# Kernel tuning notes

Hardware: AMD Instinct MI355X
Metric: run time of the kernel (lower is better)

The kernel has to match this reference:

```python
import jax, jax.numpy as jnp
import numpy as np

B, S, IN, H, NC, WSEG = 2, 256, 80, 128, 40, 64
F2 = 2 * H  # bidirectional LSTM output dim


def setup_inputs() -> dict:
    key = jax.random.key(0)
    it = iter(jax.random.split(key, 48))
    def nrm(shape, scale):
        return jax.random.normal(next(it), shape, jnp.float32) * scale
    d = {}
    d["x"] = jax.random.normal(next(it), (B, S, IN), jnp.float32)
    d["lengths"] = jnp.full((B,), S, dtype=jnp.int32)
    ins = [IN, F2]
    for l in range(2):
        for dr in ("f", "b"):
            sc = 1.0 / np.sqrt(H)
            d[f"w_ih_l{l}{dr}"] = nrm((4 * H, ins[l]), sc)
            d[f"w_hh_l{l}{dr}"] = nrm((4 * H, H), sc)
            d[f"b_l{l}{dr}"] = nrm((4 * H,), sc)
    PD = 3 * F2  # pairwise phi feature dim
    d["a_s0"] = jnp.float32(0.25); d["w_s1"] = nrm((100, PD), 1.0 / np.sqrt(PD)); d["b_s1"] = jnp.zeros((100,), jnp.float32)
    d["a_s1"] = jnp.float32(0.25); d["w_s2"] = nrm((1, 100), 0.1); d["b_s2"] = jnp.zeros((1,), jnp.float32)
    d["a_c0"] = jnp.float32(0.25); d["w_c1"] = nrm((2 * NC, F2), 1.0 / np.sqrt(F2)); d["b_c1"] = jnp.zeros((2 * NC,), jnp.float32)
    d["a_c1"] = jnp.float32(0.25); d["w_c2"] = nrm((NC, 2 * NC), 0.1); d["b_c2"] = jnp.zeros((NC,), jnp.float32)
    d["a_b0"] = jnp.float32(0.25); d["w_b1"] = nrm((2 * NC, F2), 1.0 / np.sqrt(F2)); d["b_b1"] = jnp.zeros((2 * NC,), jnp.float32)
    d["a_b1"] = jnp.float32(0.25); d["w_b2"] = nrm((2, 2 * NC), 0.1); d["b_b2"] = jnp.zeros((2,), jnp.float32)
    return d


def prelu(x, a):
    return jnp.where(x >= 0, x, a * x)


def mlp(x, a0, W1, b1, a1, W2, b2):
    h = prelu(x, a0) @ W1.T + b1
    return prelu(h, a1) @ W2.T + b2


def lstm_dir(x, Wih, Whh, b, reverse):
    # PyTorch gate order: i, f, g, o
    pre = jnp.einsum("bsi,gi->sbg", x, Wih) + b  # [S,B,4H]
    if reverse:
        pre = pre[::-1]
    h0 = jnp.zeros((x.shape[0], Whh.shape[1]), x.dtype)
    def step(carry, xt):
        h, c = carry
        g = xt + h @ Whh.T
        i, f, gg, o = jnp.split(g, 4, axis=-1)
        c = jax.nn.sigmoid(f) * c + jax.nn.sigmoid(i) * jnp.tanh(gg)
        h = jax.nn.sigmoid(o) * jnp.tanh(c)
        return (h, c), h
    _, hs = jax.lax.scan(step, (h0, h0), pre)
    if reverse:
        hs = hs[::-1]
    return jnp.swapaxes(hs, 0, 1)  # [B,S,H]


def encode(x, layers):
    out = x
    for (wif, whf, bf, wib, whb, bb) in layers:
        out = jnp.concatenate([
            lstm_dir(out, wif, whf, bf, False),
            lstm_dir(out, wib, whb, bb, True),
        ], axis=-1)
    return out


def compute_scores(rnn_out, a_s0, w_s1, b_s1, a_s1, w_s2, b_s2):
    cum = jnp.cumsum(rnn_out, axis=1)
    # phi[b,i,j] = [cum[j]-cum[i], out[i], out[j]]  (faithful to calc_phi)
    c = cum[:, None, :, :] - cum[:, :, None, :]
    sh = c.shape
    dmat = jnp.broadcast_to(rnn_out[:, :, None, :], sh)
    emat = jnp.broadcast_to(rnn_out[:, None, :, :], sh)
    phi = jnp.concatenate([c, dmat, emat], axis=-1)  # [B,S,S,3*F2]
    return mlp(phi, a_s0, w_s1, b_s1, a_s1, w_s2, b_s2)[..., 0]  # [B,S,S]


def dp_backptr(scores):
    # Viterbi-style DP: best[i] = max_{j in [i-WSEG, i)} best[j] + scores[:, j, i]
    Bn, Sn = scores.shape[:2]
    def step(best, i):
        start = jnp.maximum(0, i - WSEG)
        jidx = start + jnp.arange(WSEG)
        bwin = jax.lax.dynamic_slice(best, (0, start), (Bn, WSEG))
        swin = jax.lax.dynamic_slice(scores, (0, start, i), (Bn, WSEG, 1))[..., 0]
        cand = jnp.where(jidx[None, :] < i, bwin + swin, -1e9)
        k = (start + jnp.argmax(cand, axis=1)).astype(jnp.int32)
        best = jax.lax.dynamic_update_slice(best, jnp.max(cand, axis=1, keepdims=True), (0, i))
        return best, k
    _, ks = jax.lax.scan(step, jnp.zeros((Bn, Sn), scores.dtype), jnp.arange(1, Sn))
    backptr = jnp.concatenate([jnp.zeros((1, Bn), jnp.int32), ks], axis=0).T  # [B,S]
    return backptr


def backtrack(scores, backptr, lengths):
    Bn, Sn = scores.shape[:2]
    bar = jnp.arange(Bn)
    def step(carry, _):
        cur, acc, bm = carry
        bm = bm.at[bar, cur].set(True)
        prev = backptr[bar, cur]
        active = cur > 0
        acc = acc + jnp.where(active, scores[bar, prev, cur], 0.0)
        cur = jnp.where(active, prev, 0)
        return (cur, acc, bm), None
    init = ((lengths - 1).astype(jnp.int32), jnp.zeros((Bn,), scores.dtype), jnp.zeros((Bn, Sn), bool))
    (_, acc, bm), _ = jax.lax.scan(step, init, None, length=Sn)
    return bm, acc


def reference(x, lengths,
              w_ih_l0f, w_hh_l0f, b_l0f, w_ih_l0b, w_hh_l0b, b_l0b,
              w_ih_l1f, w_hh_l1f, b_l1f, w_ih_l1b, w_hh_l1b, b_l1b,
              a_s0, w_s1, b_s1, a_s1, w_s2, b_s2,
              a_c0, w_c1, b_c1, a_c1, w_c2, b_c2,
              a_b0, w_b1, b_b1, a_b1, w_b2, b_b2):
    layers = [
        (w_ih_l0f, w_hh_l0f, b_l0f, w_ih_l0b, w_hh_l0b, b_l0b),
        (w_ih_l1f, w_hh_l1f, b_l1f, w_ih_l1b, w_hh_l1b, b_l1b),
    ]
    rnn_out = encode(x, layers)  # [B,S,2H]
    cls_out = mlp(rnn_out, a_c0, w_c1, b_c1, a_c1, w_c2, b_c2)
    bin_out = mlp(rnn_out, a_b0, w_b1, b_b1, a_b1, w_b2, b_b2)
    scores = compute_scores(rnn_out, a_s0, w_s1, b_s1, a_s1, w_s2, b_s2)
    backptr = dp_backptr(scores)
    bmask, pred_scores = backtrack(scores, backptr, lengths)
    # bmask[b,i]==1 iff i is a predicted segment boundary (padded-dense encoding of pred lists)
    return cls_out, bin_out, bmask.astype(jnp.int32), pred_scores
```

## Files before the change

### kernel.cpp

```cpp
#include <hip/hip_runtime.h>
#include <math.h>


#define OFF_BIN 20480
#define OFF_BM  21504
#define OFF_PRED 22016

__device__ __forceinline__ float preluf(float x, float a) { return x >= 0.f ? x : a * x; }
__device__ __forceinline__ float sigf(float x) { return 1.f / (1.f + __expf(-x)); }

__global__ __launch_bounds__(256) void k_pre2(const float* __restrict__ A,
                                              const float* __restrict__ B,
                                              int Adim, int K,
                                              const float* __restrict__ wf,
                                              const float* __restrict__ bf,
                                              const float* __restrict__ wb,
                                              const float* __restrict__ bb,
                                              float* __restrict__ outF,
                                              float* __restrict__ outB) {
    __shared__ __align__(16) float xs[4 * 256];
    int r0 = blockIdx.x << 2;
    int tid = threadIdx.x;
    int Bdim = K - Adim;
    for (int e = tid; e < 4 * K; e += 256) {
        int row = e / K, kk = e - row * K;
        int tb = r0 + row; int t = tb >> 1, b = tb & 1;
        float v = (kk < Adim) ? A[(size_t)((b << 8) + t) * Adim + kk]
                              : B[(size_t)((b << 8) + t) * Bdim + (kk - Adim)];
        xs[row * K + kk] = v;
    }
    __syncthreads();
    int g = tid;
    const float* w0 = wf + (size_t)g * K;
    const float* w1 = wf + (size_t)(g + 256) * K;
    const float* w2 = wb + (size_t)g * K;
    const float* w3 = wb + (size_t)(g + 256) * K;
    float acc0[4], acc1[4], acc2[4], acc3[4];
    float b0v = bf[g], b1v = bf[g + 256], b2v = bb[g], b3v = bb[g + 256];
#pragma unroll
    for (int r = 0; r < 4; ++r) { acc0[r] = b0v; acc1[r] = b1v; acc2[r] = b2v; acc3[r] = b3v; }
    for (int k = 0; k < K; k += 4) {
        float4 wq0 = *(const float4*)(w0 + k);
        float4 wq1 = *(const float4*)(w1 + k);
        float4 wq2 = *(const float4*)(w2 + k);
        float4 wq3 = *(const float4*)(w3 + k);
#pragma unroll
        for (int r = 0; r < 4; ++r) {
            float4 xq = *(const float4*)(xs + r * K + k);
            acc0[r] += wq0.x * xq.x + wq0.y * xq.y + wq0.z * xq.z + wq0.w * xq.w;
            acc1[r] += wq1.x * xq.x + wq1.y * xq.y + wq1.z * xq.z + wq1.w * xq.w;
            acc2[r] += wq2.x * xq.x + wq2.y * xq.y + wq2.z * xq.z + wq2.w * xq.w;
            acc3[r] += wq3.x * xq.x + wq3.y * xq.y + wq3.z * xq.z + wq3.w * xq.w;
        }
    }
#pragma unroll
    for (int r = 0; r < 4; ++r) {
        int tb = r0 + r;
        outF[(size_t)tb * 512 + g]       = acc0[r];
        outF[(size_t)tb * 512 + 256 + g] = acc1[r];
        outB[(size_t)tb * 512 + g]       = acc2[r];
        outB[(size_t)tb * 512 + 256 + g] = acc3[r];
    }
}

__global__ __launch_bounds__(512, 2) void k_lstm(const float* __restrict__ pre_f,
                                                 const float* __restrict__ pre_b,
                                                 const float* __restrict__ whh_f,
                                                 const float* __restrict__ whh_b,
                                                 float* __restrict__ hout_f,
                                                 float* __restrict__ hout_b) {
    const int dir = blockIdx.x >> 1;
    const int b = blockIdx.x & 1;
    const float* pre = dir ? pre_b : pre_f;
    const float* whh = dir ? whh_b : whh_f;
    float* hout = dir ? hout_b : hout_f;
    const int tid = threadIdx.x;
    const int c = tid >> 7;
    const int gg = tid & 127;
    const int k0 = c << 5;

    float w[4][32];
#pragma unroll
    for (int j = 0; j < 4; ++j) {
#pragma unroll
        for (int k = 0; k < 32; k += 4) {
            float4 v = *(const float4*)(whh + (size_t)((j << 7) + gg) * 128 + k0 + k);
            w[j][k] = v.x; w[j][k + 1] = v.y; w[j][k + 2] = v.z; w[j][k + 3] = v.w;
        }
    }

    __shared__ float hl[128];
    __shared__ float4 part[4][128];
    if (tid < 128) hl[tid] = 0.f;
    float cst = 0.f;
    __syncthreads();

    int t0 = dir ? 255 : 0;
    float p0 = 0.f, p1 = 0.f, p2 = 0.f, p3 = 0.f;
    if (tid < 128) {
        const float* pp = pre + ((size_t)t0 * 2 + b) * 512;
        p0 = pp[gg]; p1 = pp[128 + gg]; p2 = pp[256 + gg]; p3 = pp[384 + gg];
    }

    for (int step = 0; step < 256; ++step) {
        int t = dir ? (255 - step) : step;
        float n0 = 0.f, n1 = 0.f, n2 = 0.f, n3 = 0.f;
        if (step < 255 && tid < 128) {
            int tn = dir ? (254 - step) : (step + 1);
            const float* pp = pre + ((size_t)tn * 2 + b) * 512;
            n0 = pp[gg]; n1 = pp[128 + gg]; n2 = pp[256 + gg]; n3 = pp[384 + gg];
        }
        float a0 = 0.f, a1 = 0.f, a2 = 0.f, a3 = 0.f;
#pragma unroll
        for (int k = 0; k < 32; k += 4) {
            float4 h4 = *(const float4*)(hl + k0 + k);
            a0 += w[0][k] * h4.x + w[0][k + 1] * h4.y + w[0][k + 2] * h4.z + w[0][k + 3] * h4.w;
            a1 += w[1][k] * h4.x + w[1][k + 1] * h4.y + w[1][k + 2] * h4.z + w[1][k + 3] * h4.w;
            a2 += w[2][k] * h4.x + w[2][k + 1] * h4.y + w[2][k + 2] * h4.z + w[2][k + 3] * h4.w;
            a3 += w[3][k] * h4.x + w[3][k + 1] * h4.y + w[3][k + 2] * h4.z + w[3][k + 3] * h4.w;
        }
        part[c][gg] = make_float4(a0, a1, a2, a3);
        __syncthreads();
        if (tid < 128) {
            float4 q0 = part[0][gg], q1 = part[1][gg], q2 = part[2][gg], q3 = part[3][gg];
            float gi = p0 + ((q0.x + q1.x) + (q2.x + q3.x));
            float gf = p1 + ((q0.y + q1.y) + (q2.y + q3.y));
            float gG = p2 + ((q0.z + q1.z) + (q2.z + q3.z));
            float go = p3 + ((q0.w + q1.w) + (q2.w + q3.w));
            cst = sigf(gf) * cst + sigf(gi) * tanhf(gG);
            float h = sigf(go) * tanhf(cst);
            hl[gg] = h;
            hout[(size_t)(((b << 8) + t) << 7) + gg] = h;
            p0 = n0; p1 = n1; p2 = n2; p3 = n3;
        }
        __syncthreads();
    }
}

__global__ __launch_bounds__(256) void k_cum(const float* __restrict__ h1f,
                                             const float* __restrict__ h1b,
                                             float* __restrict__ rnn,
                                             float* __restrict__ cum) {
    int b = blockIdx.x, k = threadIdx.x;
    const float* src = (k < 128) ? h1f : h1b;
    int kk = k & 127;
    float run = 0.f;
#pragma unroll 8
    for (int t = 0; t < 256; ++t) {
        float v = src[(size_t)(((b << 8) + t) << 7) + kk];
        size_t o = (size_t)(((b << 8) + t) << 8) + k;
        rnn[o] = v;
        run += v;
        cum[o] = run;
    }
}

__global__ __launch_bounds__(256) void k_pde(const float* __restrict__ rnn,
                                             const float* __restrict__ ws1,
                                             const float* __restrict__ bs1,
                                             const float* __restrict__ a_s0,
                                             float* __restrict__ Pd,
                                             float* __restrict__ Pe) {
    int row = blockIdx.x;
    __shared__ __align__(16) float pr[256];
    float a0 = a_s0[0];
    float v = rnn[(size_t)row * 256 + threadIdx.x];
    pr[threadIdx.x] = preluf(v, a0);
    __syncthreads();
    int t = threadIdx.x;
    const float4* p4 = (const float4*)pr;
    if (t < 100) {
        const float4* wr = (const float4*)(ws1 + (size_t)t * 768 + 256);
        float acc = bs1[t];
#pragma unroll 8
        for (int q = 0; q < 64; ++q) {
            float4 w4 = wr[q], x4 = p4[q];
            acc += w4.x * x4.x + w4.y * x4.y + w4.z * x4.z + w4.w * x4.w;
        }
        Pd[(size_t)row * 100 + t] = acc;
    } else if (t >= 128 && t < 228) {
        int u = t - 128;
        const float4* wr = (const float4*)(ws1 + (size_t)u * 768 + 512);
        float acc = 0.f;
#pragma unroll 8
        for (int q = 0; q < 64; ++q) {
            float4 w4 = wr[q], x4 = p4[q];
            acc += w4.x * x4.x + w4.y * x4.y + w4.z * x4.z + w4.w * x4.w;
        }
        Pe[(size_t)row * 100 + u] = acc;
    }
}

__global__ __launch_bounds__(256) void k_head(const float* __restrict__ rnn,
                                              const float* ac0p, const float* __restrict__ wc1,
                                              const float* __restrict__ bc1, const float* ac1p,
                                              const float* __restrict__ wc2, const float* __restrict__ bc2,
                                              const float* ab0p, const float* __restrict__ wb1,
                                              const float* __restrict__ bb1, const float* ab1p,
                                              const float* __restrict__ wb2, const float* __restrict__ bb2,
                                              float* __restrict__ out) {
    int row = blockIdx.x;
    int tid = threadIdx.x;
    __shared__ __align__(16) float xc[256];
    __shared__ __align__(16) float xb[256];
    __shared__ __align__(16) float hc[80];
    __shared__ __align__(16) float hb[80];
    float ac0 = ac0p[0], ac1 = ac1p[0], ab0 = ab0p[0], ab1 = ab1p[0];
    float v = rnn[(size_t)row * 256 + tid];
    xc[tid] = preluf(v, ac0);
    xb[tid] = preluf(v, ab0);
    __syncthreads();
    if (tid < 80) {
        const float4* wr = (const float4*)(wc1 + (size_t)tid * 256);
        const float4* x4 = (const float4*)xc;
        float acc = bc1[tid];
#pragma unroll 8
        for (int q = 0; q < 64; ++q) {
            float4 w4 = wr[q], p = x4[q];
            acc += w4.x * p.x + w4.y * p.y + w4.z * p.z + w4.w * p.w;
        }
        hc[tid] = preluf(acc, ac1);
    } else if (tid >= 128 && tid < 208) {
        int u = tid - 128;
        const float4* wr = (const float4*)(wb1 + (size_t)u * 256);
        const float4* x4 = (const float4*)xb;
        float acc = bb1[u];
#pragma unroll 8
        for (int q = 0; q < 64; ++q) {
            float4 w4 = wr[q], p = x4[q];
            acc += w4.x * p.x + w4.y * p.y + w4.z * p.z + w4.w * p.w;
        }
        hb[u] = preluf(acc, ab1);
    }
    __syncthreads();
    if (tid < 40) {
        const float4* wr = (const float4*)(wc2 + (size_t)tid * 80);
        const float4* h4 = (const float4*)hc;
        float acc = bc2[tid];
#pragma unroll
        for (int q = 0; q < 20; ++q) {
            float4 w4 = wr[q], p = h4[q];
            acc += w4.x * p.x + w4.y * p.y + w4.z * p.z + w4.w * p.w;
        }
        out[(size_t)row * 40 + tid] = acc;
    } else if (tid >= 64 && tid < 66) {
        int j = tid - 64;
        const float4* wr = (const float4*)(wb2 + (size_t)j * 80);
        const float4* h4 = (const float4*)hb;
        float acc = bb2[j];
#pragma unroll
        for (int q = 0; q < 20; ++q) {
            float4 w4 = wr[q], p = h4[q];
            acc += w4.x * p.x + w4.y * p.y + w4.z * p.z + w4.w * p.w;
        }
        out[OFF_BIN + (size_t)row * 2 + j] = acc;
    }
}

__global__ __launch_bounds__(256) void k_scores(const float* __restrict__ cum,
                                                const float* __restrict__ ws1,
                                                const float* __restrict__ ws2,
                                                const float* __restrict__ bs2,
                                                const float* __restrict__ Pd,
                                                const float* __restrict__ Pe,
                                                const float* a_s0p, const float* a_s1p,
                                                float* __restrict__ scT) {
    int bid = blockIdx.x;
    int dt = bid & 3, e = (bid >> 2) & 255, b = bid >> 10;
    int d0 = dt << 6;
    int tid = threadIdx.x;
    __shared__ float cume[256];
    __shared__ float Y[64 * 257];
    __shared__ float red[4][64];
    float a0 = a_s0p[0], a1 = a_s1p[0];
    cume[tid] = cum[(size_t)(((b << 8) + e) << 8) + tid];
    __syncthreads();
#pragma unroll 4
    for (int dj = 0; dj < 64; ++dj) {
        float cd = cum[(size_t)(((b << 8) + (d0 + dj)) << 8) + tid];
        Y[dj * 257 + tid] = preluf(cume[tid] - cd, a0);
    }
    __syncthreads();
    int ug = __builtin_amdgcn_readfirstlane(tid >> 6);
    int ld = tid & 63;
    int d = d0 + ld;
    float acc[25];
#pragma unroll
    for (int t = 0; t < 25; ++t) acc[t] = 0.f;
    const float* wc = ws1 + (size_t)(ug * 25) * 768;
    const float* yrow = Y + ld * 257;
    for (int k = 0; k < 256; k += 4) {
        float y0 = yrow[k], y1 = yrow[k + 1], y2 = yrow[k + 2], y3 = yrow[k + 3];
#pragma unroll
        for (int t = 0; t < 25; ++t) {
            float4 wq = *(const float4*)(wc + (size_t)t * 768 + k);
            acc[t] += y0 * wq.x + y1 * wq.y + y2 * wq.z + y3 * wq.w;
        }
    }
    const float* pdrow = Pd + (size_t)((b << 8) + d) * 100;
    const float* perow = Pe + (size_t)((b << 8) + e) * 100;
    float part = 0.f;
#pragma unroll
    for (int t = 0; t < 25; ++t) {
        int u = ug * 25 + t;
        float h = acc[t] + pdrow[u] + perow[u];
        part += preluf(h, a1) * ws2[u];
    }
    red[ug][ld] = part;
    __syncthreads();
    if (tid < 64) {
        float s = red[0][tid] + red[1][tid] + red[2][tid] + red[3][tid] + bs2[0];
        scT[(size_t)(((b << 8) + e) << 8) + d0 + tid] = s;
    }
}

__global__ __launch_bounds__(128) void k_dp(const float* __restrict__ scT,
                                            const int* __restrict__ lengths,
                                            float* __restrict__ out) {
    __shared__ float best[2][256];
    __shared__ int bp[2][256];
    __shared__ float bm[2][256];
    int tid = threadIdx.x;
    for (int i = tid; i < 512; i += 128) {
        ((float*)best)[i] = 0.f;
        ((int*)bp)[i] = 0;
        ((float*)bm)[i] = 0.f;
    }
    __syncthreads();
    int b = tid >> 6, ln = tid & 63;
    const float* sb = scT + ((size_t)b << 16);
    float sc_next = sb[(1 << 8) + ln];
    for (int i = 1; i < 256; ++i) {
        float sc = sc_next;
        if (i < 255) {
            int i2 = i + 1;
            int st2 = (i2 > 64) ? (i2 - 64) : 0;
            sc_next = sb[(i2 << 8) + st2 + ln];
        }
        int start = (i > 64) ? (i - 64) : 0;
        int j = start + ln;
        float v = -1000000000.0f;
        int ki = j;
        if (j < i) v = best[b][j] + sc;
#pragma unroll
        for (int off = 32; off > 0; off >>= 1) {
            float ov = __shfl_down(v, off);
            int ok = __shfl_down(ki, off);
            if (ov > v || (ov == v && ok < ki)) { v = ov; ki = ok; }
        }
        if (ln == 0) { best[b][i] = v; bp[b][i] = ki; }
    }
    __syncthreads();
    if (tid < 2) {
        int bb = tid;
        int cur = lengths[bb] - 1;
        out[OFF_PRED + bb] = best[bb][cur];
        for (int it = 0; it < 256; ++it) {
            bm[bb][cur] = 1.f;
            int prev = bp[bb][cur];
            cur = (cur > 0) ? prev : 0;
        }
    }
    __syncthreads();
    for (int i = tid; i < 512; i += 128) out[OFF_BM + i] = ((float*)bm)[i];
}

extern "C" void kernel_launch(void* const* d_in, const int* in_sizes, int n_in,
                              void* d_out, int out_size, void* d_ws, size_t ws_size,
                              hipStream_t stream) {
    const float* x     = (const float*)d_in[0];
    const int* lengths = (const int*)d_in[1];
    const float* wih0f = (const float*)d_in[2];
    const float* whh0f = (const float*)d_in[3];
    const float* b0f   = (const float*)d_in[4];
    const float* wih0b = (const float*)d_in[5];
    const float* whh0b = (const float*)d_in[6];
    const float* b0b   = (const float*)d_in[7];
    const float* wih1f = (const float*)d_in[8];
    const float* whh1f = (const float*)d_in[9];
    const float* b1f   = (const float*)d_in[10];
    const float* wih1b = (const float*)d_in[11];
    const float* whh1b = (const float*)d_in[12];
    const float* b1b   = (const float*)d_in[13];
    const float* a_s0  = (const float*)d_in[14];
    const float* w_s1  = (const float*)d_in[15];
    const float* b_s1  = (const float*)d_in[16];
    const float* a_s1  = (const float*)d_in[17];
    const float* w_s2  = (const float*)d_in[18];
    const float* b_s2  = (const float*)d_in[19];
    const float* a_c0  = (const float*)d_in[20];
    const float* w_c1  = (const float*)d_in[21];
    const float* b_c1  = (const float*)d_in[22];
    const float* a_c1  = (const float*)d_in[23];
    const float* w_c2  = (const float*)d_in[24];
    const float* b_c2  = (const float*)d_in[25];
    const float* a_b0  = (const float*)d_in[26];
    const float* w_b1  = (const float*)d_in[27];
    const float* b_b1  = (const float*)d_in[28];
    const float* a_b1  = (const float*)d_in[29];
    const float* w_b2  = (const float*)d_in[30];
    const float* b_b2  = (const float*)d_in[31];

    float* wsf = (float*)d_ws;
    float* preF = wsf;
    float* preB = wsf + 262144;
    float* h0f  = wsf + 524288;
    float* h0b  = wsf + 589824;
    float* h1f  = wsf + 655360;
    float* h1b  = wsf + 720896;
    float* rnn  = wsf + 786432;
    float* cum  = wsf + 917504;
    float* Pd   = wsf + 1048576;
    float* Pe   = wsf + 1099776;
    float* scT  = wsf + 1150976;
    float* out  = (float*)d_out;

    k_pre2<<<128, 256, 0, stream>>>(x, x, 80, 80, wih0f, b0f, wih0b, b0b, preF, preB);
    k_lstm<<<4, 512, 0, stream>>>(preF, preB, whh0f, whh0b, h0f, h0b);
    k_pre2<<<128, 256, 0, stream>>>(h0f, h0b, 128, 256, wih1f, b1f, wih1b, b1b, preF, preB);
    k_lstm<<<4, 512, 0, stream>>>(preF, preB, whh1f, whh1b, h1f, h1b);
    k_cum<<<2, 256, 0, stream>>>(h1f, h1b, rnn, cum);
    k_pde<<<512, 256, 0, stream>>>(rnn, w_s1, b_s1, a_s0, Pd, Pe);
    k_head<<<512, 256, 0, stream>>>(rnn, a_c0, w_c1, b_c1, a_c1, w_c2, b_c2,
                                    a_b0, w_b1, b_b1, a_b1, w_b2, b_b2, out);
    k_scores<<<2048, 256, 0, stream>>>(cum, w_s1, w_s2, b_s2, Pd, Pe, a_s0, a_s1, scT);
    k_dp<<<1, 128, 0, stream>>>(scT, lengths, out);
}
```

Baseline: 1.044 ms.

## Fuse cum/pde/head kernels into one launch and speed up LSTM gate math

Merges the cumulative-sum, pairwise-projection and classifier-head kernels into one kernel that dispatches on block index and reads the LSTM outputs directly, dropping the intermediate rnn buffer and two launches. The LSTM step now has every thread compute the gate nonlinearities redundantly, so no branch is needed, and replaces tanhf with an exp-based fast tanh. This removes launch overhead and a serial copy pass, and shortens the per-step latency of the recurrent loop. The trade-offs are redundant work in the recurrence and slightly different tanh precision.

```diff
diff --git a/kernel.cpp b/kernel.cpp
--- a/kernel.cpp
+++ b/kernel.cpp
@@ -8,6 +8,7 @@
 
 __device__ __forceinline__ float preluf(float x, float a) { return x >= 0.f ? x : a * x; }
 __device__ __forceinline__ float sigf(float x) { return 1.f / (1.f + __expf(-x)); }
+__device__ __forceinline__ float tanh_fast(float x) { return 1.f - 2.f / (__expf(2.f * x) + 1.f); }
 
 __global__ __launch_bounds__(256) void k_pre2(const float* __restrict__ A,
                                               const float* __restrict__ B,
@@ -89,23 +90,20 @@
         }
     }
 
-    __shared__ float hl[128];
+    __shared__ __align__(16) float hl[128];
     __shared__ float4 part[4][128];
     if (tid < 128) hl[tid] = 0.f;
     float cst = 0.f;
     __syncthreads();
 
     int t0 = dir ? 255 : 0;
-    float p0 = 0.f, p1 = 0.f, p2 = 0.f, p3 = 0.f;
-    if (tid < 128) {
-        const float* pp = pre + ((size_t)t0 * 2 + b) * 512;
-        p0 = pp[gg]; p1 = pp[128 + gg]; p2 = pp[256 + gg]; p3 = pp[384 + gg];
-    }
+    const float* pp0 = pre + ((size_t)t0 * 2 + b) * 512;
+    float p0 = pp0[gg], p1 = pp0[128 + gg], p2 = pp0[256 + gg], p3 = pp0[384 + gg];
 
     for (int step = 0; step < 256; ++step) {
         int t = dir ? (255 - step) : step;
         float n0 = 0.f, n1 = 0.f, n2 = 0.f, n3 = 0.f;
-        if (step < 255 && tid < 128) {
+        if (step < 255) {
             int tn = dir ? (254 - step) : (step + 1);
             const float* pp = pre + ((size_t)tn * 2 + b) * 512;
             n0 = pp[gg]; n1 = pp[128 + gg]; n2 = pp[256 + gg]; n3 = pp[384 + gg];
@@ -121,139 +119,131 @@
         }
         part[c][gg] = make_float4(a0, a1, a2, a3);
         __syncthreads();
-        if (tid < 128) {
-            float4 q0 = part[0][gg], q1 = part[1][gg], q2 = part[2][gg], q3 = part[3][gg];
-            float gi = p0 + ((q0.x + q1.x) + (q2.x + q3.x));
-            float gf = p1 + ((q0.y + q1.y) + (q2.y + q3.y));
-            float gG = p2 + ((q0.z + q1.z) + (q2.z + q3.z));
-            float go = p3 + ((q0.w + q1.w) + (q2.w + q3.w));
-            cst = sigf(gf) * cst + sigf(gi) * tanhf(gG);
-            float h = sigf(go) * tanhf(cst);
-            hl[gg] = h;
-            hout[(size_t)(((b << 8) + t) << 7) + gg] = h;
-            p0 = n0; p1 = n1; p2 = n2; p3 = n3;
-        }
+        float4 q0 = part[0][gg], q1 = part[1][gg], q2 = part[2][gg], q3 = part[3][gg];
+        float gi = p0 + ((q0.x + q1.x) + (q2.x + q3.x));
+        float gf = p1 + ((q0.y + q1.y) + (q2.y + q3.y));
+        float gG = p2 + ((q0.z + q1.z) + (q2.z + q3.z));
+        float go = p3 + ((q0.w + q1.w) + (q2.w + q3.w));
+        cst = sigf(gf) * cst + sigf(gi) * tanh_fast(gG);
+        float h = sigf(go) * tanh_fast(cst);
+        hl[gg] = h;
+        if (tid < 128) hout[(size_t)(((b << 8) + t) << 7) + gg] = h;
+        p0 = n0; p1 = n1; p2 = n2; p3 = n3;
         __syncthreads();
     }
 }
 
-__global__ __launch_bounds__(256) void k_cum(const float* __restrict__ h1f,
-                                             const float* __restrict__ h1b,
-                                             float* __restrict__ rnn,
-                                             float* __restrict__ cum) {
-    int b = blockIdx.x, k = threadIdx.x;
-    const float* src = (k < 128) ? h1f : h1b;
-    int kk = k & 127;
-    float run = 0.f;
-#pragma unroll 8
-    for (int t = 0; t < 256; ++t) {
-        float v = src[(size_t)(((b << 8) + t) << 7) + kk];
-        size_t o = (size_t)(((b << 8) + t) << 8) + k;
-        rnn[o] = v;
-        run += v;
-        cum[o] = run;
-    }
-}
-
-__global__ __launch_bounds__(256) void k_pde(const float* __restrict__ rnn,
-                                             const float* __restrict__ ws1,
-                                             const float* __restrict__ bs1,
-                                             const float* __restrict__ a_s0,
-                                             float* __restrict__ Pd,
-                                             float* __restrict__ Pe) {
-    int row = blockIdx.x;
-    __shared__ __align__(16) float pr[256];
-    float a0 = a_s0[0];
-    float v = rnn[(size_t)row * 256 + threadIdx.x];
-    pr[threadIdx.x] = preluf(v, a0);
-    __syncthreads();
-    int t = threadIdx.x;
-    const float4* p4 = (const float4*)pr;
-    if (t < 100) {
-        const float4* wr = (const float4*)(ws1 + (size_t)t * 768 + 256);
-        float acc = bs1[t];
-#pragma unroll 8
-        for (int q = 0; q < 64; ++q) {
-            float4 w4 = wr[q], x4 = p4[q];
-            acc += w4.x * x4.x + w4.y * x4.y + w4.z * x4.z + w4.w * x4.w;
-        }
-        Pd[(size_t)row * 100 + t] = acc;
-    } else if (t >= 128 && t < 228) {
-        int u = t - 128;
-        const float4* wr = (const float4*)(ws1 + (size_t)u * 768 + 512);
-        float acc = 0.f;
-#pragma unroll 8
-        for (int q = 0; q < 64; ++q) {
-            float4 w4 = wr[q], x4 = p4[q];
-            acc += w4.x * x4.x + w4.y * x4.y + w4.z * x4.z + w4.w * x4.w;
-        }
-        Pe[(size_t)row * 100 + u] = acc;
-    }
-}
-
-__global__ __launch_bounds__(256) void k_head(const float* __restrict__ rnn,
-                                              const float* ac0p, const float* __restrict__ wc1,
-                                              const float* __restrict__ bc1, const float* ac1p,
-                                              const float* __restrict__ wc2, const float* __restrict__ bc2,
-                                              const float* ab0p, const float* __restrict__ wb1,
-                                              const float* __restrict__ bb1, const float* ab1p,
-                                              const float* __restrict__ wb2, const float* __restrict__ bb2,
-                                              float* __restrict__ out) {
-    int row = blockIdx.x;
-    int tid = threadIdx.x;
-    __shared__ __align__(16) float xc[256];
-    __shared__ __align__(16) float xb[256];
+__global__ __launch_bounds__(256) void k_feats(const float* __restrict__ h1f,
+                                               const float* __restrict__ h1b,
+                                               const float* __restrict__ ws1,
+                                               const float* __restrict__ bs1,
+                                               const float* a_s0,
+                                               float* __restrict__ Pd,
+                                               float* __restrict__ Pe,
+                                               const float* ac0p, const float* __restrict__ wc1,
+                                               const float* __restrict__ bc1, const float* ac1p,
+                                               const float* __restrict__ wc2, const float* __restrict__ bc2,
+                                               const float* ab0p, const float* __restrict__ wb1,
+                                               const float* __restrict__ bb1, const float* ab1p,
+                                               const float* __restrict__ wb2, const float* __restrict__ bb2,
+                                               float* __restrict__ out,
+                                               float* __restrict__ cum) {
+    __shared__ __align__(16) float xa[256];
+    __shared__ __align__(16) float xb2[256];
     __shared__ __align__(16) float hc[80];
     __shared__ __align__(16) float hb[80];
-    float ac0 = ac0p[0], ac1 = ac1p[0], ab0 = ab0p[0], ab1 = ab1p[0];
-    float v = rnn[(size_t)row * 256 + tid];
-    xc[tid] = preluf(v, ac0);
-    xb[tid] = preluf(v, ab0);
-    __syncthreads();
-    if (tid < 80) {
-        const float4* wr = (const float4*)(wc1 + (size_t)tid * 256);
-        const float4* x4 = (const float4*)xc;
-        float acc = bc1[tid];
+    int bid = blockIdx.x;
+    int tid = threadIdx.x;
+    int kk = tid & 127;
+    if (bid < 512) {
+        int row = bid;
+        float a0 = a_s0[0];
+        float v = ((tid < 128) ? h1f : h1b)[(size_t)row * 128 + kk];
+        xa[tid] = preluf(v, a0);
+        __syncthreads();
+        const float4* p4 = (const float4*)xa;
+        if (tid < 100) {
+            const float4* wr = (const float4*)(ws1 + (size_t)tid * 768 + 256);
+            float acc = bs1[tid];
 #pragma unroll 8
-        for (int q = 0; q < 64; ++q) {
-            float4 w4 = wr[q], p = x4[q];
-            acc += w4.x * p.x + w4.y * p.y + w4.z * p.z + w4.w * p.w;
-        }
-        hc[tid] = preluf(acc, ac1);
-    } else if (tid >= 128 && tid < 208) {
-        int u = tid - 128;
-        const float4* wr = (const float4*)(wb1 + (size_t)u * 256);
-        const float4* x4 = (const float4*)xb;
-        float acc = bb1[u];
+            for (int q = 0; q < 64; ++q) {
+                float4 w4 = wr[q], x4 = p4[q];
+                acc += w4.x * x4.x + w4.y * x4.y + w4.z * x4.z + w4.w * x4.w;
+            }
+            Pd[(size_t)row * 100 + tid] = acc;
+        } else if (tid >= 128 && tid < 228) {
+            int u = tid - 128;
+            const float4* wr = (const float4*)(ws1 + (size_t)u * 768 + 512);
+            float acc = 0.f;
 #pragma unroll 8
-        for (int q = 0; q < 64; ++q) {
-            float4 w4 = wr[q], p = x4[q];
-            acc += w4.x * p.x + w4.y * p.y + w4.z * p.z + w4.w * p.w;
-        }
-        hb[u] = preluf(acc, ab1);
-    }
-    __syncthreads();
-    if (tid < 40) {
-        const float4* wr = (const float4*)(wc2 + (size_t)tid * 80);
-        const float4* h4 = (const float4*)hc;
-        float acc = bc2[tid];
-#pragma unroll
-        for (int q = 0; q < 20; ++q) {
-            float4 w4 = wr[q], p = h4[q];
-            acc += w4.x * p.x + w4.y * p.y + w4.z * p.z + w4.w * p.w;
-        }
-        out[(size_t)row * 40 + tid] = acc;
-    } else if (tid >= 64 && tid < 66) {
-        int j = tid - 64;
-        const float4* wr = (const float4*)(wb2 + (size_t)j * 80);
-        const float4* h4 = (const float4*)hb;
-        float acc = bb2[j];
-#pragma unroll
-        for (int q = 0; q < 20; ++q) {
-            float4 w4 = wr[q], p = h4[q];
-            acc += w4.x * p.x + w4.y * p.y + w4.z * p.z + w4.w * p.w;
-        }
-        out[OFF_BIN + (size_t)row * 2 + j] = acc;
+            for (int q = 0; q < 64; ++q) {
+                float4 w4 = wr[q], x4 = p4[q];
+                acc += w4.x * x4.x + w4.y * x4.y + w4.z * x4.z + w4.w * x4.w;
+            }
+            Pe[(size_t)row * 100 + u] = acc;
+        }
+    } else if (bid < 1024) {
+        int row = bid - 512;
+        float ac0 = ac0p[0], ac1 = ac1p[0], ab0 = ab0p[0], ab1 = ab1p[0];
+        float v = ((tid < 128) ? h1f : h1b)[(size_t)row * 128 + kk];
+        xa[tid] = preluf(v, ac0);
+        xb2[tid] = preluf(v, ab0);
+        __syncthreads();
+        if (tid < 80) {
+            const float4* wr = (const float4*)(wc1 + (size_t)tid * 256);
+            const float4* x4 = (const float4*)xa;
+            float acc = bc1[tid];
+#pragma unroll 8
+            for (int q = 0; q < 64; ++q) {
+                float4 w4 = wr[q], p = x4[q];
+                acc += w4.x * p.x + w4.y * p.y + w4.z * p.z + w4.w * p.w;
+            }
+            hc[tid] = preluf(acc, ac1);
+        } else if (tid >= 128 && tid < 208) {
+            int u = tid - 128;
+            const float4* wr = (const float4*)(wb1 + (size_t)u * 256);
+            const float4* x4 = (const float4*)xb2;
+            float acc = bb1[u];
+#pragma unroll 8
+            for (int q = 0; q < 64; ++q) {
+                float4 w4 = wr[q], p = x4[q];
+                acc += w4.x * p.x + w4.y * p.y + w4.z * p.z + w4.w * p.w;
+            }
+            hb[u] = preluf(acc, ab1);
+        }
+        __syncthreads();
+        if (tid < 40) {
+            const float4* wr = (const float4*)(wc2 + (size_t)tid * 80);
+            const float4* h4 = (const float4*)hc;
+            float acc = bc2[tid];
+#pragma unroll
+            for (int q = 0; q < 20; ++q) {
+                float4 w4 = wr[q], p = h4[q];
+                acc += w4.x * p.x + w4.y * p.y + w4.z * p.z + w4.w * p.w;
+            }
+            out[(size_t)row * 40 + tid] = acc;
+        } else if (tid >= 64 && tid < 66) {
+            int j = tid - 64;
+            const float4* wr = (const float4*)(wb2 + (size_t)j * 80);
+            const float4* h4 = (const float4*)hb;
+            float acc = bb2[j];
+#pragma unroll
+            for (int q = 0; q < 20; ++q) {
+                float4 w4 = wr[q], p = h4[q];
+                acc += w4.x * p.x + w4.y * p.y + w4.z * p.z + w4.w * p.w;
+            }
+            out[OFF_BIN + (size_t)row * 2 + j] = acc;
+        }
+    } else {
+        int b = bid - 1024;
+        const float* src = (tid < 128) ? h1f : h1b;
+        float run = 0.f;
+#pragma unroll 8
+        for (int t = 0; t < 256; ++t) {
+            float v = src[(size_t)(((b << 8) + t) << 7) + kk];
+            cum[(size_t)(((b << 8) + t) << 8) + tid] = run + v;
+            run += v;
+        }
     }
 }
 
@@ -408,21 +398,19 @@
     float* h0b  = wsf + 589824;
     float* h1f  = wsf + 655360;
     float* h1b  = wsf + 720896;
-    float* rnn  = wsf + 786432;
-    float* cum  = wsf + 917504;
-    float* Pd   = wsf + 1048576;
-    float* Pe   = wsf + 1099776;
-    float* scT  = wsf + 1150976;
+    float* cum  = wsf + 786432;
+    float* Pd   = wsf + 917504;
+    float* Pe   = wsf + 968704;
+    float* scT  = wsf + 1019904;
     float* out  = (float*)d_out;
 
     k_pre2<<<128, 256, 0, stream>>>(x, x, 80, 80, wih0f, b0f, wih0b, b0b, preF, preB);
     k_lstm<<<4, 512, 0, stream>>>(preF, preB, whh0f, whh0b, h0f, h0b);
     k_pre2<<<128, 256, 0, stream>>>(h0f, h0b, 128, 256, wih1f, b1f, wih1b, b1b, preF, preB);
     k_lstm<<<4, 512, 0, stream>>>(preF, preB, whh1f, whh1b, h1f, h1b);
-    k_cum<<<2, 256, 0, stream>>>(h1f, h1b, rnn, cum);
-    k_pde<<<512, 256, 0, stream>>>(rnn, w_s1, b_s1, a_s0, Pd, Pe);
-    k_head<<<512, 256, 0, stream>>>(rnn, a_c0, w_c1, b_c1, a_c1, w_c2, b_c2,
-                                    a_b0, w_b1, b_b1, a_b1, w_b2, b_b2, out);
+    k_feats<<<1026, 256, 0, stream>>>(h1f, h1b, w_s1, b_s1, a_s0, Pd, Pe,
+                                      a_c0, w_c1, b_c1, a_c1, w_c2, b_c2,
+                                      a_b0, w_b1, b_b1, a_b1, w_b2, b_b2, out, cum);
     k_scores<<<2048, 256, 0, stream>>>(cum, w_s1, w_s2, b_s2, Pd, Pe, a_s0, a_s1, scT);
     k_dp<<<1, 128, 0, stream>>>(scT, lengths, out);
 }
```

New measurement: 1.053 ms. About the same (+0.9%).
